# Optimization experiments

Hardware: AMD Instinct MI355X
Metric: run time of the kernel (lower is better)

The kernel has to match this reference:

```python
import jax, jax.numpy as jnp
import numpy as np

EMBED_DIM = 1024
NUM_HEADS = 16
HEAD_DIM = EMBED_DIM // NUM_HEADS
T, B = 2048, 2


def setup_inputs() -> dict:
    key = jax.random.key(0)
    ks = jax.random.split(key, 12)
    s = 1.0 / np.sqrt(EMBED_DIM)
    x = jax.random.normal(ks[0], (T, B, EMBED_DIM), dtype=jnp.float32)
    time_decay = jax.random.uniform(ks[1], (T, B, 1), dtype=jnp.float32)
    # causal mask: masked_fill where mask == 0
    attn_mask = jnp.tril(jnp.ones((T, T), dtype=jnp.int32))
    Wq = jax.random.uniform(ks[2], (EMBED_DIM, EMBED_DIM), jnp.float32, -s, s)
    bq = jax.random.uniform(ks[3], (EMBED_DIM,), jnp.float32, -s, s)
    Wk = jax.random.uniform(ks[4], (EMBED_DIM, EMBED_DIM), jnp.float32, -s, s)
    bk = jax.random.uniform(ks[5], (EMBED_DIM,), jnp.float32, -s, s)
    Wv = jax.random.uniform(ks[6], (EMBED_DIM, EMBED_DIM), jnp.float32, -s, s)
    bv = jax.random.uniform(ks[7], (EMBED_DIM,), jnp.float32, -s, s)
    Wo = jax.random.uniform(ks[8], (EMBED_DIM, EMBED_DIM), jnp.float32, -s, s)
    bo = jax.random.uniform(ks[9], (EMBED_DIM,), jnp.float32, -s, s)
    return {"x": x, "time_decay": time_decay, "attn_mask": attn_mask,
            "Wq": Wq, "bq": bq, "Wk": Wk, "bk": bk,
            "Wv": Wv, "bv": bv, "Wo": Wo, "bo": bo}


def reference(x, time_decay, attn_mask, Wq, bq, Wk, bk, Wv, bv, Wo, bo):
    t, b, e = x.shape
    h, d = NUM_HEADS, HEAD_DIM
    # linear (torch: y = x @ W.T + b), then split heads -> (B, H, T, D)
    def proj(W, bias):
        y = jnp.einsum('tbe,fe->tbf', x, W) + bias
        return y.reshape(t, b, h, d).transpose(1, 2, 0, 3)
    Q, K, V = proj(Wq, bq), proj(Wk, bk), proj(Wv, bv)
    scores = jnp.einsum('bhqd,bhkd->bhqk', Q, K) / np.sqrt(d).astype(jnp.float32)
    scores = jnp.where(attn_mask == 0, jnp.float32(-1e9), scores)
    attn = jax.nn.softmax(scores, axis=-1)
    out = jnp.einsum('bhqk,bhkd->bhqd', attn, V)      # (B,H,T,D)
    out = out.transpose(2, 0, 1, 3).reshape(t, b, e)   # (T,B,E)
    out = jnp.einsum('tbe,fe->tbf', out, Wo) + bo
    return out * time_decay
```

## Files before the change

kernel.cpp:

```cpp
#include <hip/hip_runtime.h>


typedef unsigned short u16;
typedef unsigned int u32;
typedef __attribute__((ext_vector_type(8))) short bf16x8_t;
typedef __attribute__((ext_vector_type(4))) float fx4_t;

#define T_SEQ 2048
#define BATCH 2
#define EMB   1024
#define NH    16
#define HD    64
#define MROWS (T_SEQ * BATCH)

#define EXP2F(x) __builtin_amdgcn_exp2f(x)

__device__ __forceinline__ float bf2f(u16 u) {
  union { unsigned int i; float f; } v;
  v.i = ((unsigned int)u) << 16;
  return v.f;
}
__device__ __forceinline__ u16 f2bf(float f) {
  union { float f; unsigned int i; } v;
  v.f = f;
  unsigned int x = v.i;
  unsigned int r = (x + 0x7fffu + ((x >> 16) & 1u)) >> 16;
  return (u16)r;
}
__device__ __forceinline__ u32 fbits(float f) {
  union { float f; u32 i; } v; v.f = f; return v.i;
}

__device__ __forceinline__ void glds16(const void* g, void* l) {
  __builtin_amdgcn_global_load_lds(
      (const __attribute__((address_space(1))) unsigned int*)g,
      (__attribute__((address_space(3))) unsigned int*)l, 16, 0, 0);
}


__global__ void cvt_all(const float* __restrict__ x,
                        const float* __restrict__ wq, const float* __restrict__ wk,
                        const float* __restrict__ wv, const float* __restrict__ wo,
                        u16* __restrict__ xb,
                        u16* __restrict__ wqb, u16* __restrict__ wkb,
                        u16* __restrict__ wvb, u16* __restrict__ wob) {
  int i = blockIdx.x * blockDim.x + threadIdx.x;
  const float* src; u16* dst; int off;
  if (i < 1048576)      { src = x;  dst = xb;  off = i; }
  else if (i < 1310720) { src = wq; dst = wqb; off = i - 1048576; }
  else if (i < 1572864) { src = wk; dst = wkb; off = i - 1310720; }
  else if (i < 1835008) { src = wv; dst = wvb; off = i - 1572864; }
  else                  { src = wo; dst = wob; off = i - 1835008; }
  float4 v = ((const float4*)src)[off];
  ushort4 o;
  o.x = f2bf(v.x); o.y = f2bf(v.y); o.z = f2bf(v.z); o.w = f2bf(v.w);
  ((ushort4*)dst)[off] = o;
}

__global__ __launch_bounds__(256, 2) void gemm_qkv(
    const u16* __restrict__ xb,
    const u16* __restrict__ wq, const u16* __restrict__ wk, const u16* __restrict__ wv,
    const float* __restrict__ bq, const float* __restrict__ bk, const float* __restrict__ bv,
    u16* __restrict__ Qm, u16* __restrict__ Km, u16* __restrict__ VTg) {
  __shared__ short As[2][128 * 64];
  __shared__ short Bs[2][128 * 64];

  const int z = blockIdx.z;
  const u16* W = (z == 0) ? wq : (z == 1) ? wk : wv;
  const float* bias = (z == 0) ? bq : (z == 1) ? bk : bv;

  const int tid = threadIdx.x;
  const int bm = blockIdx.x, bn = blockIdx.y;
  const int lane = tid & 63, w = tid >> 6;
  const int wm = w >> 1, wn = w & 1;
  const int lr = lane & 15, quad = lane >> 4;
  const int r0 = lane >> 3;
  const int c8s = ((lane & 7) ^ r0) * 8;
  const int sw = (lr & 7);

  fx4_t acc[4][4];
#pragma unroll
  for (int i = 0; i < 4; i++)
#pragma unroll
    for (int j = 0; j < 4; j++) acc[i][j] = (fx4_t){0.f, 0.f, 0.f, 0.f};

#define STAGE(kt_, bi_)                                                          \
  {                                                                              \
    const int k0_ = (kt_) * 64;                                                  \
    _Pragma("unroll")                                                            \
    for (int i = 0; i < 4; i++) {                                                \
      const int rr = w * 32 + i * 8;                                             \
      const int ml = bm * 128 + rr + r0;                                         \
      const int grow = (z == 2) ? (((ml & 2047) << 1) | (ml >> 11)) : ml;        \
      glds16(xb + (size_t)grow * EMB + k0_ + c8s, &As[bi_][rr * 64]);            \
      glds16(W + (size_t)(bn * 128 + rr + r0) * EMB + k0_ + c8s,                 \
             &Bs[bi_][rr * 64]);                                                 \
    }                                                                            \
  }

  const int nkt = EMB / 64;
  STAGE(0, 0);
  __syncthreads();

  for (int kt = 0; kt < nkt; kt++) {
    const int buf = kt & 1;
    if (kt + 1 < nkt) STAGE(kt + 1, buf ^ 1);
#pragma unroll
    for (int ks = 0; ks < 2; ++ks) {
      bf16x8_t a[4], b[4];
#pragma unroll
      for (int i = 0; i < 4; i++)
        a[i] = *(const bf16x8_t*)&As[buf][(wm * 64 + i * 16 + lr) * 64 + (((ks * 4 + quad) ^ sw) * 8)];
#pragma unroll
      for (int j = 0; j < 4; j++)
        b[j] = *(const bf16x8_t*)&Bs[buf][(wn * 64 + j * 16 + lr) * 64 + (((ks * 4 + quad) ^ sw) * 8)];
      if (z == 2) {
#pragma unroll
        for (int i = 0; i < 4; i++)
#pragma unroll
          for (int j = 0; j < 4; j++)
            acc[i][j] = __builtin_amdgcn_mfma_f32_16x16x32_bf16(b[j], a[i], acc[i][j], 0, 0, 0);
      } else {
#pragma unroll
        for (int i = 0; i < 4; i++)
#pragma unroll
          for (int j = 0; j < 4; j++)
            acc[i][j] = __builtin_amdgcn_mfma_f32_16x16x32_bf16(a[i], b[j], acc[i][j], 0, 0, 0);
      }
    }
    __syncthreads();
  }
#undef STAGE

  if (z == 2) {
#pragma unroll
    for (int i = 0; i < 4; i++) {
#pragma unroll
      for (int j = 0; j < 4; j++) {
#pragma unroll
        for (int r = 0; r < 4; r++) {
          const int n = bn * 128 + wn * 64 + j * 16 + quad * 4 + r;
          const int ml = bm * 128 + wm * 64 + i * 16 + lr;
          const int t = ml & 2047, bb = ml >> 11;
          const int h = n >> 6, d = n & 63;
          VTg[((size_t)(bb * NH + h) * HD + d) * T_SEQ + t] = f2bf(acc[i][j][r] + bias[n]);
        }
      }
    }
  } else {
    u16* dst = (z == 0) ? Qm : Km;
#pragma unroll
    for (int i = 0; i < 4; i++) {
#pragma unroll
      for (int j = 0; j < 4; j++) {
        const int n = bn * 128 + wn * 64 + j * 16 + lr;
        const float bsv = bias[n];
#pragma unroll
        for (int r = 0; r < 4; r++) {
          const int m = bm * 128 + wm * 64 + i * 16 + quad * 4 + r;
          dst[(size_t)m * EMB + n] = f2bf(acc[i][j][r] + bsv);
        }
      }
    }
  }
}

__global__ __launch_bounds__(256, 2) void gemm_out(
    const u16* __restrict__ Ob, const u16* __restrict__ wo,
    const float* __restrict__ bo, const float* __restrict__ td,
    float* __restrict__ out) {
  __shared__ short As[64 * 64];
  __shared__ short Bs[128 * 64];

  const int tid = threadIdx.x;
  const int bm = blockIdx.x, bn = blockIdx.y;
  const int lane = tid & 63, w = tid >> 6;
  const int wm = w >> 1, wn = w & 1;
  const int lr = lane & 15, quad = lane >> 4;
  const int r0 = lane >> 3;
  const int c8s = ((lane & 7) ^ r0) * 8;
  const int sw = (lr & 7);

  fx4_t acc[2][4];
#pragma unroll
  for (int i = 0; i < 2; i++)
#pragma unroll
    for (int j = 0; j < 4; j++) acc[i][j] = (fx4_t){0.f, 0.f, 0.f, 0.f};

  for (int k0 = 0; k0 < EMB; k0 += 64) {
#pragma unroll
    for (int i = 0; i < 2; i++) {
      const int rr = w * 16 + i * 8;
      glds16(Ob + (size_t)(bm * 64 + rr + r0) * EMB + k0 + c8s, &As[rr * 64]);
    }
#pragma unroll
    for (int i = 0; i < 4; i++) {
      const int rr = w * 32 + i * 8;
      glds16(wo + (size_t)(bn * 128 + rr + r0) * EMB + k0 + c8s, &Bs[rr * 64]);
    }
    __syncthreads();
#pragma unroll
    for (int ks = 0; ks < 2; ++ks) {
      bf16x8_t a[2], b[4];
#pragma unroll
      for (int i = 0; i < 2; i++)
        a[i] = *(const bf16x8_t*)&As[(wm * 32 + i * 16 + lr) * 64 + (((ks * 4 + quad) ^ sw) * 8)];
#pragma unroll
      for (int j = 0; j < 4; j++)
        b[j] = *(const bf16x8_t*)&Bs[(wn * 64 + j * 16 + lr) * 64 + (((ks * 4 + quad) ^ sw) * 8)];
#pragma unroll
      for (int i = 0; i < 2; i++)
#pragma unroll
        for (int j = 0; j < 4; j++)
          acc[i][j] = __builtin_amdgcn_mfma_f32_16x16x32_bf16(a[i], b[j], acc[i][j], 0, 0, 0);
    }
    __syncthreads();
  }

#pragma unroll
  for (int i = 0; i < 2; i++) {
#pragma unroll
    for (int j = 0; j < 4; j++) {
      const int n = bn * 128 + wn * 64 + j * 16 + lr;
      const float bsv = bo[n];
#pragma unroll
      for (int r = 0; r < 4; r++) {
        const int m = bm * 64 + wm * 32 + i * 16 + quad * 4 + r;
        out[(size_t)m * EMB + n] = (acc[i][j][r] + bsv) * td[m];
      }
    }
  }
}

__global__ __launch_bounds__(256, 3) void attn_mfma8(
    const u16* __restrict__ Qm, const u16* __restrict__ Km, const u16* __restrict__ VTg,
    u16* __restrict__ Ob) {
  __shared__ short Kd[2][64 * 64];
  __shared__ short Vd[2][64 * 64];
  __shared__ short Ps[4][16 * 72];

  const int blk = blockIdx.x;
  const int bh = blk & 31;
  const int j = blk >> 5;
  const int qt = (j & 1) ? (31 - (j >> 1)) : (j >> 1);
  const int qb = qt * 64;
  const int b = bh >> 4, h = bh & 15;

  const int tid = threadIdx.x;
  const int w = tid >> 6, lane = tid & 63;
  const int lr = lane & 15, quad = lane >> 4;
  const int r0 = lane >> 3;
  const int c8s = ((lane & 7) ^ r0) * 8;
  const int sw = (lr & 7);

  const u16* Qbase = Qm + (size_t)b * EMB + (size_t)h * HD;
  const u16* Kbase = Km + (size_t)b * EMB + (size_t)h * HD;
  const u16* VTb = VTg + (size_t)bh * HD * T_SEQ;

  const float QSCALE = 0.18033688f;
  bf16x8_t qf[2];
#pragma unroll
  for (int ks = 0; ks < 2; ks++) {
    bf16x8_t v = *(const bf16x8_t*)(Qbase + (size_t)(qb + w * 16 + lr) * 2 * EMB + ks * 32 + quad * 8);
    bf16x8_t o;
#pragma unroll
    for (int e = 0; e < 8; e++) o[e] = (short)f2bf(bf2f((u16)v[e]) * QSCALE);
    qf[ks] = o;
  }

  fx4_t acc_o[4];
#pragma unroll
  for (int dn = 0; dn < 4; dn++) acc_o[dn] = (fx4_t){0.f, 0.f, 0.f, 0.f};
  float l_par = 0.f;

#define STAGE(kt_, buf_)                                                            \
  {                                                                                 \
    const int k0_ = (kt_) * 64;                                                     \
    _Pragma("unroll")                                                               \
    for (int i = 0; i < 2; i++) {                                                   \
      const int rr = w * 16 + i * 8;                                                \
      glds16(Kbase + (size_t)(k0_ + rr + r0) * 2 * EMB + c8s, &Kd[buf_][rr * 64]);  \
      glds16(VTb + (size_t)(rr + r0) * T_SEQ + k0_ + c8s, &Vd[buf_][rr * 64]);      \
    }                                                                               \
  }

  const int nkt = qt + 1;
  STAGE(0, 0);
  __syncthreads();

  for (int kt = 0; kt < nkt; kt++) {
    const int buf = kt & 1;
    if (kt + 1 < nkt) STAGE(kt + 1, buf ^ 1);

    fx4_t st[4];
#pragma unroll
    for (int nt = 0; nt < 4; nt++) st[nt] = (fx4_t){0.f, 0.f, 0.f, 0.f};
#pragma unroll
    for (int ks = 0; ks < 2; ks++) {
#pragma unroll
      for (int nt = 0; nt < 4; nt++) {
        bf16x8_t kf = *(const bf16x8_t*)&Kd[buf][(nt * 16 + lr) * 64 + (((ks * 4 + quad) ^ sw) * 8)];
        st[nt] = __builtin_amdgcn_mfma_f32_16x16x32_bf16(kf, qf[ks], st[nt], 0, 0, 0);
      }
    }

    bf16x8_t vf[2][4];
#pragma unroll
    for (int ks = 0; ks < 2; ks++)
#pragma unroll
      for (int dn = 0; dn < 4; dn++)
        vf[ks][dn] = *(const bf16x8_t*)&Vd[buf][(dn * 16 + lr) * 64 + (((ks * 4 + quad) ^ sw) * 8)];

    if (kt == qt) {
#pragma unroll
      for (int nt = 0; nt < 4; nt++)
#pragma unroll
        for (int r = 0; r < 4; r++)
          if (nt * 16 + quad * 4 + r > w * 16 + lr) st[nt][r] = -1e30f;
    }

    short* Pw = Ps[w];
#pragma unroll
    for (int nt = 0; nt < 4; nt++) {
      float e0 = EXP2F(st[nt][0]);
      float e1 = EXP2F(st[nt][1]);
      float e2 = EXP2F(st[nt][2]);
      float e3 = EXP2F(st[nt][3]);
      u32 p01 = (fbits(e0) >> 16) | (fbits(e1) & 0xFFFF0000u);
      u32 p23 = (fbits(e2) >> 16) | (fbits(e3) & 0xFFFF0000u);
      uint2 pv; pv.x = p01; pv.y = p23;
      *(uint2*)&Pw[lr * 72 + nt * 16 + quad * 4] = pv;
      l_par += (e0 + e1) + (e2 + e3);
    }

#pragma unroll
    for (int ks = 0; ks < 2; ks++) {
      bf16x8_t pf = *(const bf16x8_t*)&Pw[lr * 72 + ks * 32 + quad * 8];
#pragma unroll
      for (int dn = 0; dn < 4; dn++)
        acc_o[dn] = __builtin_amdgcn_mfma_f32_16x16x32_bf16(pf, vf[ks][dn], acc_o[dn], 0, 0, 0);
    }

    __syncthreads();
  }
#undef STAGE

  l_par += __shfl_xor(l_par, 16);
  l_par += __shfl_xor(l_par, 32);
  const float inv = 1.0f / l_par;
#pragma unroll
  for (int r = 0; r < 4; r++) {
    const float inv_r = __shfl(inv, quad * 4 + r);
    const int t = qb + w * 16 + quad * 4 + r;
#pragma unroll
    for (int dn = 0; dn < 4; dn++) {
      const int d = dn * 16 + lr;
      Ob[(size_t)(t * BATCH + b) * EMB + h * HD + d] = f2bf(acc_o[dn][r] * inv_r);
    }
  }
}

extern "C" void kernel_launch(void* const* d_in, const int* in_sizes, int n_in,
                              void* d_out, int out_size, void* d_ws, size_t ws_size,
                              hipStream_t stream) {
  const float* x  = (const float*)d_in[0];
  const float* td = (const float*)d_in[1];
  const float* Wq = (const float*)d_in[3];
  const float* bq = (const float*)d_in[4];
  const float* Wk = (const float*)d_in[5];
  const float* bk = (const float*)d_in[6];
  const float* Wv = (const float*)d_in[7];
  const float* bv = (const float*)d_in[8];
  const float* Wo = (const float*)d_in[9];
  const float* bo = (const float*)d_in[10];
  float* out = (float*)d_out;

  char* ws = (char*)d_ws;
  u16* xb  = (u16*)(ws + 0);
  u16* wqb = (u16*)(ws + ((size_t)8  << 20));
  u16* wkb = (u16*)(ws + ((size_t)10 << 20));
  u16* wvb = (u16*)(ws + ((size_t)12 << 20));
  u16* wob = (u16*)(ws + ((size_t)14 << 20));
  u16* Qm  = (u16*)(ws + ((size_t)16 << 20));
  u16* Km  = (u16*)(ws + ((size_t)24 << 20));
  u16* VTg = (u16*)(ws + ((size_t)32 << 20));
  u16* Ob  = xb;

  cvt_all<<<8192, 256, 0, stream>>>(x, Wq, Wk, Wv, Wo, xb, wqb, wkb, wvb, wob);

  gemm_qkv<<<dim3(MROWS / 128, EMB / 128, 3), 256, 0, stream>>>(
      xb, wqb, wkb, wvb, bq, bk, bv, Qm, Km, VTg);

  attn_mfma8<<<1024, 256, 0, stream>>>(Qm, Km, VTg, Ob);

  gemm_out<<<dim3(MROWS / 64, EMB / 128), 256, 0, stream>>>(Ob, wob, bo, td, out);
}
```

Measured before the change: 192.6 us.

## Fuse all four stages into one cooperative persistent kernel with grid syncs

Merges the convert, QKV GEMM, attention and output GEMM stages into a single cooperative kernel of 768 blocks, with grid.sync between stages. The four separate launches and their inter-kernel gaps go away. Attention work is re-mapped so the first 256 blocks each take a pair of short and long causal tiles, balancing the load. The cost is less parallelism per stage (768 blocks versus up to 8192 for convert), grid-sync overhead, and some blocks idling in the output GEMM. If the cooperative launch fails, it falls back to the original four-kernel path.

```diff
diff --git a/kernel.cpp b/kernel.cpp
--- a/kernel.cpp
+++ b/kernel.cpp
@@ -1,4 +1,7 @@
 #include <hip/hip_runtime.h>
+#include <hip/hip_cooperative_groups.h>
+
+namespace cg = cooperative_groups;
 
 
 typedef unsigned short u16;
@@ -35,6 +38,353 @@
   __builtin_amdgcn_global_load_lds(
       (const __attribute__((address_space(1))) unsigned int*)g,
       (__attribute__((address_space(3))) unsigned int*)l, 16, 0, 0);
+}
+
+
+
+__device__ __forceinline__ void cvt_body(
+    int gstride,
+    const float* __restrict__ x,
+    const float* __restrict__ wq, const float* __restrict__ wk,
+    const float* __restrict__ wv, const float* __restrict__ wo,
+    u16* __restrict__ xb, u16* __restrict__ wqb, u16* __restrict__ wkb,
+    u16* __restrict__ wvb, u16* __restrict__ wob) {
+  for (int i = blockIdx.x * blockDim.x + threadIdx.x; i < 2097152; i += gstride) {
+    const float* src; u16* dst; int off;
+    if (i < 1048576)      { src = x;  dst = xb;  off = i; }
+    else if (i < 1310720) { src = wq; dst = wqb; off = i - 1048576; }
+    else if (i < 1572864) { src = wk; dst = wkb; off = i - 1310720; }
+    else if (i < 1835008) { src = wv; dst = wvb; off = i - 1572864; }
+    else                  { src = wo; dst = wob; off = i - 1835008; }
+    float4 v = ((const float4*)src)[off];
+    ushort4 o;
+    o.x = f2bf(v.x); o.y = f2bf(v.y); o.z = f2bf(v.z); o.w = f2bf(v.w);
+    ((ushort4*)dst)[off] = o;
+  }
+}
+
+__device__ __forceinline__ void qkv_body(
+    short* As, short* Bs, int bm, int bn, int z,
+    const u16* __restrict__ xb,
+    const u16* __restrict__ wq, const u16* __restrict__ wk, const u16* __restrict__ wv,
+    const float* __restrict__ bq, const float* __restrict__ bk, const float* __restrict__ bv,
+    u16* __restrict__ Qm, u16* __restrict__ Km, u16* __restrict__ VTg) {
+  const u16* W = (z == 0) ? wq : (z == 1) ? wk : wv;
+  const float* bias = (z == 0) ? bq : (z == 1) ? bk : bv;
+
+  const int tid = threadIdx.x;
+  const int lane = tid & 63, w = tid >> 6;
+  const int wm = w >> 1, wn = w & 1;
+  const int lr = lane & 15, quad = lane >> 4;
+  const int r0 = lane >> 3;
+  const int c8s = ((lane & 7) ^ r0) * 8;
+  const int sw = (lr & 7);
+
+  fx4_t acc[4][4];
+#pragma unroll
+  for (int i = 0; i < 4; i++)
+#pragma unroll
+    for (int j = 0; j < 4; j++) acc[i][j] = (fx4_t){0.f, 0.f, 0.f, 0.f};
+
+  for (int k0 = 0; k0 < EMB; k0 += 64) {
+#pragma unroll
+    for (int i = 0; i < 4; i++) {
+      const int rr = w * 32 + i * 8;
+      const int ml = bm * 128 + rr + r0;
+      const int grow = (z == 2) ? (((ml & 2047) << 1) | (ml >> 11)) : ml;
+      glds16(xb + (size_t)grow * EMB + k0 + c8s, &As[rr * 64]);
+      glds16(W + (size_t)(bn * 128 + rr + r0) * EMB + k0 + c8s, &Bs[rr * 64]);
+    }
+    __syncthreads();
+#pragma unroll
+    for (int ks = 0; ks < 2; ++ks) {
+      bf16x8_t a[4], b[4];
+#pragma unroll
+      for (int i = 0; i < 4; i++)
+        a[i] = *(const bf16x8_t*)&As[(wm * 64 + i * 16 + lr) * 64 + (((ks * 4 + quad) ^ sw) * 8)];
+#pragma unroll
+      for (int j = 0; j < 4; j++)
+        b[j] = *(const bf16x8_t*)&Bs[(wn * 64 + j * 16 + lr) * 64 + (((ks * 4 + quad) ^ sw) * 8)];
+      if (z == 2) {
+#pragma unroll
+        for (int i = 0; i < 4; i++)
+#pragma unroll
+          for (int j = 0; j < 4; j++)
+            acc[i][j] = __builtin_amdgcn_mfma_f32_16x16x32_bf16(b[j], a[i], acc[i][j], 0, 0, 0);
+      } else {
+#pragma unroll
+        for (int i = 0; i < 4; i++)
+#pragma unroll
+          for (int j = 0; j < 4; j++)
+            acc[i][j] = __builtin_amdgcn_mfma_f32_16x16x32_bf16(a[i], b[j], acc[i][j], 0, 0, 0);
+      }
+    }
+    __syncthreads();
+  }
+
+  if (z == 2) {
+#pragma unroll
+    for (int i = 0; i < 4; i++) {
+#pragma unroll
+      for (int j = 0; j < 4; j++) {
+#pragma unroll
+        for (int r = 0; r < 4; r++) {
+          const int n = bn * 128 + wn * 64 + j * 16 + quad * 4 + r;
+          const int ml = bm * 128 + wm * 64 + i * 16 + lr;
+          const int t = ml & 2047, bb = ml >> 11;
+          const int h = n >> 6, d = n & 63;
+          VTg[((size_t)(bb * NH + h) * HD + d) * T_SEQ + t] = f2bf(acc[i][j][r] + bias[n]);
+        }
+      }
+    }
+  } else {
+    u16* dst = (z == 0) ? Qm : Km;
+#pragma unroll
+    for (int i = 0; i < 4; i++) {
+#pragma unroll
+      for (int j = 0; j < 4; j++) {
+        const int n = bn * 128 + wn * 64 + j * 16 + lr;
+        const float bsv = bias[n];
+#pragma unroll
+        for (int r = 0; r < 4; r++) {
+          const int m = bm * 128 + wm * 64 + i * 16 + quad * 4 + r;
+          dst[(size_t)m * EMB + n] = f2bf(acc[i][j][r] + bsv);
+        }
+      }
+    }
+  }
+}
+
+__device__ __forceinline__ void attn_body(
+    short* Kd, short* Vd, short* Ps, int qt, int bh,
+    const u16* __restrict__ Qm, const u16* __restrict__ Km,
+    const u16* __restrict__ VTg, u16* __restrict__ Ob) {
+  const int qb = qt * 64;
+  const int b = bh >> 4, h = bh & 15;
+
+  const int tid = threadIdx.x;
+  const int w = tid >> 6, lane = tid & 63;
+  const int lr = lane & 15, quad = lane >> 4;
+  const int r0 = lane >> 3;
+  const int c8s = ((lane & 7) ^ r0) * 8;
+  const int sw = (lr & 7);
+
+  const u16* Qbase = Qm + (size_t)b * EMB + (size_t)h * HD;
+  const u16* Kbase = Km + (size_t)b * EMB + (size_t)h * HD;
+  const u16* VTb = VTg + (size_t)bh * HD * T_SEQ;
+
+  const float QSCALE = 0.18033688f;
+  bf16x8_t qf[2];
+#pragma unroll
+  for (int ks = 0; ks < 2; ks++) {
+    bf16x8_t v = *(const bf16x8_t*)(Qbase + (size_t)(qb + w * 16 + lr) * 2 * EMB + ks * 32 + quad * 8);
+    bf16x8_t o;
+#pragma unroll
+    for (int e = 0; e < 8; e++) o[e] = (short)f2bf(bf2f((u16)v[e]) * QSCALE);
+    qf[ks] = o;
+  }
+
+  fx4_t acc_o[4];
+#pragma unroll
+  for (int dn = 0; dn < 4; dn++) acc_o[dn] = (fx4_t){0.f, 0.f, 0.f, 0.f};
+  float l_par = 0.f;
+
+#define ASTG(kt_, buf_)                                                                  \
+  {                                                                                      \
+    const int k0_ = (kt_) * 64;                                                          \
+    _Pragma("unroll")                                                                    \
+    for (int i = 0; i < 2; i++) {                                                        \
+      const int rr = w * 16 + i * 8;                                                     \
+      glds16(Kbase + (size_t)(k0_ + rr + r0) * 2 * EMB + c8s, &Kd[(buf_)*4096 + rr*64]); \
+      glds16(VTb + (size_t)(rr + r0) * T_SEQ + k0_ + c8s, &Vd[(buf_)*4096 + rr*64]);     \
+    }                                                                                    \
+  }
+
+  const int nkt = qt + 1;
+  ASTG(0, 0);
+  __syncthreads();
+
+  for (int kt = 0; kt < nkt; kt++) {
+    const int buf = kt & 1;
+    if (kt + 1 < nkt) ASTG(kt + 1, buf ^ 1);
+
+    fx4_t st[4];
+#pragma unroll
+    for (int nt = 0; nt < 4; nt++) st[nt] = (fx4_t){0.f, 0.f, 0.f, 0.f};
+#pragma unroll
+    for (int ks = 0; ks < 2; ks++) {
+#pragma unroll
+      for (int nt = 0; nt < 4; nt++) {
+        bf16x8_t kf = *(const bf16x8_t*)&Kd[buf*4096 + (nt * 16 + lr) * 64 + (((ks * 4 + quad) ^ sw) * 8)];
+        st[nt] = __builtin_amdgcn_mfma_f32_16x16x32_bf16(kf, qf[ks], st[nt], 0, 0, 0);
+      }
+    }
+
+    bf16x8_t vf[2][4];
+#pragma unroll
+    for (int ks = 0; ks < 2; ks++)
+#pragma unroll
+      for (int dn = 0; dn < 4; dn++)
+        vf[ks][dn] = *(const bf16x8_t*)&Vd[buf*4096 + (dn * 16 + lr) * 64 + (((ks * 4 + quad) ^ sw) * 8)];
+
+    if (kt == qt) {
+#pragma unroll
+      for (int nt = 0; nt < 4; nt++)
+#pragma unroll
+        for (int r = 0; r < 4; r++)
+          if (nt * 16 + quad * 4 + r > w * 16 + lr) st[nt][r] = -1e30f;
+    }
+
+    short* Pw = Ps + w * (16 * 72);
+#pragma unroll
+    for (int nt = 0; nt < 4; nt++) {
+      float e0 = EXP2F(st[nt][0]);
+      float e1 = EXP2F(st[nt][1]);
+      float e2 = EXP2F(st[nt][2]);
+      float e3 = EXP2F(st[nt][3]);
+      u32 p01 = (fbits(e0) >> 16) | (fbits(e1) & 0xFFFF0000u);
+      u32 p23 = (fbits(e2) >> 16) | (fbits(e3) & 0xFFFF0000u);
+      uint2 pv; pv.x = p01; pv.y = p23;
+      *(uint2*)&Pw[lr * 72 + nt * 16 + quad * 4] = pv;
+      l_par += (e0 + e1) + (e2 + e3);
+    }
+
+#pragma unroll
+    for (int ks = 0; ks < 2; ks++) {
+      bf16x8_t pf = *(const bf16x8_t*)&Pw[lr * 72 + ks * 32 + quad * 8];
+#pragma unroll
+      for (int dn = 0; dn < 4; dn++)
+        acc_o[dn] = __builtin_amdgcn_mfma_f32_16x16x32_bf16(pf, vf[ks][dn], acc_o[dn], 0, 0, 0);
+    }
+
+    __syncthreads();
+  }
+#undef ASTG
+
+  l_par += __shfl_xor(l_par, 16);
+  l_par += __shfl_xor(l_par, 32);
+  const float inv = 1.0f / l_par;
+#pragma unroll
+  for (int r = 0; r < 4; r++) {
+    const float inv_r = __shfl(inv, quad * 4 + r);
+    const int t = qb + w * 16 + quad * 4 + r;
+#pragma unroll
+    for (int dn = 0; dn < 4; dn++) {
+      const int d = dn * 16 + lr;
+      Ob[(size_t)(t * BATCH + b) * EMB + h * HD + d] = f2bf(acc_o[dn][r] * inv_r);
+    }
+  }
+}
+
+__device__ __forceinline__ void out_body(
+    short* As, short* Bs, int bm, int bn,
+    const u16* __restrict__ Ob, const u16* __restrict__ wo,
+    const float* __restrict__ bo, const float* __restrict__ td,
+    float* __restrict__ out) {
+  const int tid = threadIdx.x;
+  const int lane = tid & 63, w = tid >> 6;
+  const int wm = w >> 1, wn = w & 1;
+  const int lr = lane & 15, quad = lane >> 4;
+  const int r0 = lane >> 3;
+  const int c8s = ((lane & 7) ^ r0) * 8;
+  const int sw = (lr & 7);
+
+  fx4_t acc[2][4];
+#pragma unroll
+  for (int i = 0; i < 2; i++)
+#pragma unroll
+    for (int j = 0; j < 4; j++) acc[i][j] = (fx4_t){0.f, 0.f, 0.f, 0.f};
+
+  for (int k0 = 0; k0 < EMB; k0 += 64) {
+#pragma unroll
+    for (int i = 0; i < 2; i++) {
+      const int rr = w * 16 + i * 8;
+      glds16(Ob + (size_t)(bm * 64 + rr + r0) * EMB + k0 + c8s, &As[rr * 64]);
+    }
+#pragma unroll
+    for (int i = 0; i < 4; i++) {
+      const int rr = w * 32 + i * 8;
+      glds16(wo + (size_t)(bn * 128 + rr + r0) * EMB + k0 + c8s, &Bs[rr * 64]);
+    }
+    __syncthreads();
+#pragma unroll
+    for (int ks = 0; ks < 2; ++ks) {
+      bf16x8_t a[2], b[4];
+#pragma unroll
+      for (int i = 0; i < 2; i++)
+        a[i] = *(const bf16x8_t*)&As[(wm * 32 + i * 16 + lr) * 64 + (((ks * 4 + quad) ^ sw) * 8)];
+#pragma unroll
+      for (int j = 0; j < 4; j++)
+        b[j] = *(const bf16x8_t*)&Bs[(wn * 64 + j * 16 + lr) * 64 + (((ks * 4 + quad) ^ sw) * 8)];
+#pragma unroll
+      for (int i = 0; i < 2; i++)
+#pragma unroll
+        for (int j = 0; j < 4; j++)
+          acc[i][j] = __builtin_amdgcn_mfma_f32_16x16x32_bf16(a[i], b[j], acc[i][j], 0, 0, 0);
+    }
+    __syncthreads();
+  }
+
+#pragma unroll
+  for (int i = 0; i < 2; i++) {
+#pragma unroll
+    for (int j = 0; j < 4; j++) {
+      const int n = bn * 128 + wn * 64 + j * 16 + lr;
+      const float bsv = bo[n];
+#pragma unroll
+      for (int r = 0; r < 4; r++) {
+        const int m = bm * 64 + wm * 32 + i * 16 + quad * 4 + r;
+        out[(size_t)m * EMB + n] = (acc[i][j][r] + bsv) * td[m];
+      }
+    }
+  }
+}
+
+__global__ __launch_bounds__(256, 3) void fused_all(
+    const float* __restrict__ x, const float* __restrict__ td,
+    const float* __restrict__ Wq, const float* __restrict__ bq,
+    const float* __restrict__ Wk, const float* __restrict__ bk,
+    const float* __restrict__ Wv, const float* __restrict__ bv,
+    const float* __restrict__ Wo, const float* __restrict__ bo,
+    u16* __restrict__ xb, u16* __restrict__ wqb, u16* __restrict__ wkb,
+    u16* __restrict__ wvb, u16* __restrict__ wob,
+    u16* __restrict__ Qm, u16* __restrict__ Km, u16* __restrict__ VTg,
+    float* __restrict__ out) {
+  __shared__ union {
+    struct { short As[128 * 64]; short Bs[128 * 64]; } q;
+    struct { short Kd[2 * 64 * 64]; short Vd[2 * 64 * 64]; short Ps[4 * 16 * 72]; } a;
+    struct { short As[64 * 64]; short Bs[128 * 64]; } o;
+  } lds;
+
+  cg::grid_group grid = cg::this_grid();
+  const int blk = blockIdx.x;
+
+  cvt_body(768 * 256, x, Wq, Wk, Wv, Wo, xb, wqb, wkb, wvb, wob);
+  grid.sync();
+
+  {
+    const int z = blk >> 8, r = blk & 255;
+    qkv_body(lds.q.As, lds.q.Bs, r & 31, r >> 5, z,
+             xb, wqb, wkb, wvb, bq, bk, bv, Qm, Km, VTg);
+  }
+  grid.sync();
+
+  u16* Ob = xb;
+  {
+    const int nj = (blk < 256) ? 2 : 1;
+    for (int jj = 0; jj < nj; jj++) {
+      int qt, bh;
+      if (blk < 256) { qt = jj ? (15 - (blk >> 5)) : (blk >> 5); bh = blk & 31; }
+      else           { qt = 16 + ((blk - 256) >> 5);             bh = (blk - 256) & 31; }
+      attn_body(lds.a.Kd, lds.a.Vd, lds.a.Ps, qt, bh, Qm, Km, VTg, Ob);
+      __syncthreads();
+    }
+  }
+  grid.sync();
+
+  if (blk < 512) {
+    out_body(lds.o.As, lds.o.Bs, blk & 63, blk >> 6, Ob, wob, bo, td, out);
+  }
 }
 
 
@@ -171,193 +521,21 @@
     float* __restrict__ out) {
   __shared__ short As[64 * 64];
   __shared__ short Bs[128 * 64];
-
-  const int tid = threadIdx.x;
-  const int bm = blockIdx.x, bn = blockIdx.y;
-  const int lane = tid & 63, w = tid >> 6;
-  const int wm = w >> 1, wn = w & 1;
-  const int lr = lane & 15, quad = lane >> 4;
-  const int r0 = lane >> 3;
-  const int c8s = ((lane & 7) ^ r0) * 8;
-  const int sw = (lr & 7);
-
-  fx4_t acc[2][4];
-#pragma unroll
-  for (int i = 0; i < 2; i++)
-#pragma unroll
-    for (int j = 0; j < 4; j++) acc[i][j] = (fx4_t){0.f, 0.f, 0.f, 0.f};
-
-  for (int k0 = 0; k0 < EMB; k0 += 64) {
-#pragma unroll
-    for (int i = 0; i < 2; i++) {
-      const int rr = w * 16 + i * 8;
-      glds16(Ob + (size_t)(bm * 64 + rr + r0) * EMB + k0 + c8s, &As[rr * 64]);
-    }
-#pragma unroll
-    for (int i = 0; i < 4; i++) {
-      const int rr = w * 32 + i * 8;
-      glds16(wo + (size_t)(bn * 128 + rr + r0) * EMB + k0 + c8s, &Bs[rr * 64]);
-    }
-    __syncthreads();
-#pragma unroll
-    for (int ks = 0; ks < 2; ++ks) {
-      bf16x8_t a[2], b[4];
-#pragma unroll
-      for (int i = 0; i < 2; i++)
-        a[i] = *(const bf16x8_t*)&As[(wm * 32 + i * 16 + lr) * 64 + (((ks * 4 + quad) ^ sw) * 8)];
-#pragma unroll
-      for (int j = 0; j < 4; j++)
-        b[j] = *(const bf16x8_t*)&Bs[(wn * 64 + j * 16 + lr) * 64 + (((ks * 4 + quad) ^ sw) * 8)];
-#pragma unroll
-      for (int i = 0; i < 2; i++)
-#pragma unroll
-        for (int j = 0; j < 4; j++)
-          acc[i][j] = __builtin_amdgcn_mfma_f32_16x16x32_bf16(a[i], b[j], acc[i][j], 0, 0, 0);
-    }
-    __syncthreads();
-  }
-
-#pragma unroll
-  for (int i = 0; i < 2; i++) {
-#pragma unroll
-    for (int j = 0; j < 4; j++) {
-      const int n = bn * 128 + wn * 64 + j * 16 + lr;
-      const float bsv = bo[n];
-#pragma unroll
-      for (int r = 0; r < 4; r++) {
-        const int m = bm * 64 + wm * 32 + i * 16 + quad * 4 + r;
-        out[(size_t)m * EMB + n] = (acc[i][j][r] + bsv) * td[m];
-      }
-    }
-  }
+  out_body(As, Bs, blockIdx.x, blockIdx.y, Ob, wo, bo, td, out);
 }
 
 __global__ __launch_bounds__(256, 3) void attn_mfma8(
     const u16* __restrict__ Qm, const u16* __restrict__ Km, const u16* __restrict__ VTg,
     u16* __restrict__ Ob) {
-  __shared__ short Kd[2][64 * 64];
-  __shared__ short Vd[2][64 * 64];
-  __shared__ short Ps[4][16 * 72];
+  __shared__ short Kd[2 * 64 * 64];
+  __shared__ short Vd[2 * 64 * 64];
+  __shared__ short Ps[4 * 16 * 72];
 
   const int blk = blockIdx.x;
   const int bh = blk & 31;
   const int j = blk >> 5;
   const int qt = (j & 1) ? (31 - (j >> 1)) : (j >> 1);
-  const int qb = qt * 64;
-  const int b = bh >> 4, h = bh & 15;
-
-  const int tid = threadIdx.x;
-  const int w = tid >> 6, lane = tid & 63;
-  const int lr = lane & 15, quad = lane >> 4;
-  const int r0 = lane >> 3;
-  const int c8s = ((lane & 7) ^ r0) * 8;
-  const int sw = (lr & 7);
-
-  const u16* Qbase = Qm + (size_t)b * EMB + (size_t)h * HD;
-  const u16* Kbase = Km + (size_t)b * EMB + (size_t)h * HD;
-  const u16* VTb = VTg + (size_t)bh * HD * T_SEQ;
-
-  const float QSCALE = 0.18033688f;
-  bf16x8_t qf[2];
-#pragma unroll
-  for (int ks = 0; ks < 2; ks++) {
-    bf16x8_t v = *(const bf16x8_t*)(Qbase + (size_t)(qb + w * 16 + lr) * 2 * EMB + ks * 32 + quad * 8);
-    bf16x8_t o;
-#pragma unroll
-    for (int e = 0; e < 8; e++) o[e] = (short)f2bf(bf2f((u16)v[e]) * QSCALE);
-    qf[ks] = o;
-  }
-
-  fx4_t acc_o[4];
-#pragma unroll
-  for (int dn = 0; dn < 4; dn++) acc_o[dn] = (fx4_t){0.f, 0.f, 0.f, 0.f};
-  float l_par = 0.f;
-
-#define STAGE(kt_, buf_)                                                            \
-  {                                                                                 \
-    const int k0_ = (kt_) * 64;                                                     \
-    _Pragma("unroll")                                                               \
-    for (int i = 0; i < 2; i++) {                                                   \
-      const int rr = w * 16 + i * 8;                                                \
-      glds16(Kbase + (size_t)(k0_ + rr + r0) * 2 * EMB + c8s, &Kd[buf_][rr * 64]);  \
-      glds16(VTb + (size_t)(rr + r0) * T_SEQ + k0_ + c8s, &Vd[buf_][rr * 64]);      \
-    }                                                                               \
-  }
-
-  const int nkt = qt + 1;
-  STAGE(0, 0);
-  __syncthreads();
-
-  for (int kt = 0; kt < nkt; kt++) {
-    const int buf = kt & 1;
-    if (kt + 1 < nkt) STAGE(kt + 1, buf ^ 1);
-
-    fx4_t st[4];
-#pragma unroll
-    for (int nt = 0; nt < 4; nt++) st[nt] = (fx4_t){0.f, 0.f, 0.f, 0.f};
-#pragma unroll
-    for (int ks = 0; ks < 2; ks++) {
-#pragma unroll
-      for (int nt = 0; nt < 4; nt++) {
-        bf16x8_t kf = *(const bf16x8_t*)&Kd[buf][(nt * 16 + lr) * 64 + (((ks * 4 + quad) ^ sw) * 8)];
-        st[nt] = __builtin_amdgcn_mfma_f32_16x16x32_bf16(kf, qf[ks], st[nt], 0, 0, 0);
-      }
-    }
-
-    bf16x8_t vf[2][4];
-#pragma unroll
-    for (int ks = 0; ks < 2; ks++)
-#pragma unroll
-      for (int dn = 0; dn < 4; dn++)
-        vf[ks][dn] = *(const bf16x8_t*)&Vd[buf][(dn * 16 + lr) * 64 + (((ks * 4 + quad) ^ sw) * 8)];
-
-    if (kt == qt) {
-#pragma unroll
-      for (int nt = 0; nt < 4; nt++)
-#pragma unroll
-        for (int r = 0; r < 4; r++)
-          if (nt * 16 + quad * 4 + r > w * 16 + lr) st[nt][r] = -1e30f;
-    }
-
-    short* Pw = Ps[w];
-#pragma unroll
-    for (int nt = 0; nt < 4; nt++) {
-      float e0 = EXP2F(st[nt][0]);
-      float e1 = EXP2F(st[nt][1]);
-      float e2 = EXP2F(st[nt][2]);
-      float e3 = EXP2F(st[nt][3]);
-      u32 p01 = (fbits(e0) >> 16) | (fbits(e1) & 0xFFFF0000u);
-      u32 p23 = (fbits(e2) >> 16) | (fbits(e3) & 0xFFFF0000u);
-      uint2 pv; pv.x = p01; pv.y = p23;
-      *(uint2*)&Pw[lr * 72 + nt * 16 + quad * 4] = pv;
-      l_par += (e0 + e1) + (e2 + e3);
-    }
-
-#pragma unroll
-    for (int ks = 0; ks < 2; ks++) {
-      bf16x8_t pf = *(const bf16x8_t*)&Pw[lr * 72 + ks * 32 + quad * 8];
-#pragma unroll
-      for (int dn = 0; dn < 4; dn++)
-        acc_o[dn] = __builtin_amdgcn_mfma_f32_16x16x32_bf16(pf, vf[ks][dn], acc_o[dn], 0, 0, 0);
-    }
-
-    __syncthreads();
-  }
-#undef STAGE
-
-  l_par += __shfl_xor(l_par, 16);
-  l_par += __shfl_xor(l_par, 32);
-  const float inv = 1.0f / l_par;
-#pragma unroll
-  for (int r = 0; r < 4; r++) {
-    const float inv_r = __shfl(inv, quad * 4 + r);
-    const int t = qb + w * 16 + quad * 4 + r;
-#pragma unroll
-    for (int dn = 0; dn < 4; dn++) {
-      const int d = dn * 16 + lr;
-      Ob[(size_t)(t * BATCH + b) * EMB + h * HD + d] = f2bf(acc_o[dn][r] * inv_r);
-    }
-  }
+  attn_body(Kd, Vd, Ps, qt, bh, Qm, Km, VTg, Ob);
 }
 
 extern "C" void kernel_launch(void* const* d_in, const int* in_sizes, int n_in,
@@ -386,12 +564,21 @@
   u16* VTg = (u16*)(ws + ((size_t)32 << 20));
   u16* Ob  = xb;
 
-  cvt_all<<<8192, 256, 0, stream>>>(x, Wq, Wk, Wv, Wo, xb, wqb, wkb, wvb, wob);
-
-  gemm_qkv<<<dim3(MROWS / 128, EMB / 128, 3), 256, 0, stream>>>(
-      xb, wqb, wkb, wvb, bq, bk, bv, Qm, Km, VTg);
-
-  attn_mfma8<<<1024, 256, 0, stream>>>(Qm, Km, VTg, Ob);
-
-  gemm_out<<<dim3(MROWS / 64, EMB / 128), 256, 0, stream>>>(Ob, wob, bo, td, out);
-}
+  void* kargs[] = {
+      (void*)&x,  (void*)&td,
+      (void*)&Wq, (void*)&bq, (void*)&Wk, (void*)&bk,
+      (void*)&Wv, (void*)&bv, (void*)&Wo, (void*)&bo,
+      (void*)&xb, (void*)&wqb, (void*)&wkb, (void*)&wvb, (void*)&wob,
+      (void*)&Qm, (void*)&Km, (void*)&VTg, (void*)&out};
+  hipError_t err = hipLaunchCooperativeKernel(
+      (const void*)fused_all, dim3(768), dim3(256), kargs, 0, stream);
+
+  if (err != hipSuccess) {
+    (void)hipGetLastError();
+    cvt_all<<<8192, 256, 0, stream>>>(x, Wq, Wk, Wv, Wo, xb, wqb, wkb, wvb, wob);
+    gemm_qkv<<<dim3(MROWS / 128, EMB / 128, 3), 256, 0, stream>>>(
+        xb, wqb, wkb, wvb, bq, bk, bv, Qm, Km, VTg);
+    attn_mfma8<<<1024, 256, 0, stream>>>(Qm, Km, VTg, Ob);
+    gemm_out<<<dim3(MROWS / 64, EMB / 128), 256, 0, stream>>>(Ob, wob, bo, td, out);
+  }
+}
```

Measured after the change: 556.5 us. +189.0%, slower.
